# Kernel tuning notes

Measured on AMD Instinct MI355X. Metric: run time of the kernel, lower is better.

## Reference

```python
import jax, jax.numpy as jnp
import numpy as np

USER_NUM = 50000
ITEM_NUM = 50000
N = USER_NUM + ITEM_NUM
VT_DIM = 512
CAT_NUM = 1000
CAT_DIM = 32
HIDDEN = 128
OUT = 64
E = 2_000_000
BAG = 5


def setup_inputs() -> dict:
    key = jax.random.key(0)
    ks = jax.random.split(key, 12)
    inp = {
        "vt_feature": jax.random.normal(ks[0], (ITEM_NUM, VT_DIM), jnp.float32),
        "cat_indices": jax.random.randint(ks[1], (ITEM_NUM * BAG,), 0, CAT_NUM),
        "cat_offsets": jnp.arange(ITEM_NUM) * BAG,
        "edge_index": jax.random.randint(ks[2], (2, E), 0, N),
        # learned parameters
        "cat_table": jax.random.normal(ks[3], (CAT_NUM, CAT_DIM), jnp.float32) * 0.1,
        "fuse_w": jax.random.normal(ks[4], (HIDDEN, VT_DIM + CAT_DIM), jnp.float32) * (1.0 / np.sqrt(VT_DIM + CAT_DIM)),
        "user": jax.random.normal(ks[5], (USER_NUM, HIDDEN), jnp.float32) * 0.1,
        "w1_l": jax.random.normal(ks[6], (HIDDEN, HIDDEN), jnp.float32) * (1.0 / np.sqrt(HIDDEN)),
        "b1": jnp.zeros((HIDDEN,), jnp.float32),
        "w1_r": jax.random.normal(ks[7], (HIDDEN, HIDDEN), jnp.float32) * (1.0 / np.sqrt(HIDDEN)),
        "w2_l": jax.random.normal(ks[8], (OUT, HIDDEN), jnp.float32) * (1.0 / np.sqrt(HIDDEN)),
        "b2": jnp.zeros((OUT,), jnp.float32),
        "w2_r": jax.random.normal(ks[9], (OUT, HIDDEN), jnp.float32) * (1.0 / np.sqrt(HIDDEN)),
    }
    return inp


def _embedding_bag_mean(table, indices, offsets, num_bags):
    # EmbeddingBag(mode='mean') with offsets: segment-mean of table lookups.
    pos = jnp.arange(indices.shape[0])
    seg = jnp.searchsorted(offsets, pos, side="right") - 1  # bag id per index
    sums = jax.ops.segment_sum(table[indices], seg, num_segments=num_bags)
    cnt = jax.ops.segment_sum(jnp.ones_like(pos, jnp.float32), seg, num_segments=num_bags)
    return sums / jnp.maximum(cnt, 1.0)[:, None]


def _sage_conv(x, edge_index, w_l, b_l, w_r):
    # PyG SAGEConv (aggr='mean'): lin_l(mean_{j->i} x_j) + lin_r(x_i)
    src, dst = edge_index[0], edge_index[1]
    agg = jax.ops.segment_sum(x[src], dst, num_segments=N)
    deg = jax.ops.segment_sum(jnp.ones((src.shape[0],), x.dtype), dst, num_segments=N)
    agg = agg / jnp.maximum(deg, 1.0)[:, None]
    return agg @ w_l.T + b_l + x @ w_r.T


def reference(vt_feature, cat_indices, cat_offsets, edge_index, cat_table,
              fuse_w, user, w1_l, b1, w1_r, w2_l, b2, w2_r):
    cat_emb = _embedding_bag_mean(cat_table, cat_indices, cat_offsets, ITEM_NUM)
    item_feat = jnp.concatenate([vt_feature, cat_emb], axis=1) @ fuse_w.T
    x0 = jnp.concatenate([user, item_feat], axis=0)  # [N, hidden]
    x1 = jax.nn.leaky_relu(_sage_conv(x0, edge_index, w1_l, b1, w1_r), negative_slope=0.01)
    # dropout is identity in eval mode
    x2 = _sage_conv(x1, edge_index, w2_l, b2, w2_r)
    return x2
```

## Files before the change

### kernel.cpp

```cpp
#include <hip/hip_runtime.h>

#define USER_N   50000
#define ITEM_N   50000
#define NNODE    100000
#define VT_DIM   512
#define CAT_DIM  32
#define HIDDEN   128
#define OUTD     64
#define PADCAP   64

#define BINC    8192
#define NBKT    98
#define BSHIFT  10
#define SLICES  8

typedef __attribute__((ext_vector_type(8))) short short8;
typedef __attribute__((ext_vector_type(4))) float f32x4;

__device__ __forceinline__ float bf2f(unsigned short u) {
    return __uint_as_float(((unsigned int)u) << 16);
}
__device__ __forceinline__ unsigned short f2bf(float f) {
    unsigned int u = __float_as_uint(f);
    unsigned int r = u + 0x7fffu + ((u >> 16) & 1u);
    return (unsigned short)(r >> 16);
}

__global__ __launch_bounds__(256) void k_catemb(const float* __restrict__ cat_table,
                                                const int* __restrict__ cat_idx,
                                                const int* __restrict__ cat_off,
                                                unsigned short* __restrict__ catemb,
                                                int item_num, int total_idx) {
    int gid = blockIdx.x * 256 + threadIdx.x;
    int item = gid >> 5;
    int d = gid & 31;
    if (item >= item_num) return;
    int s = cat_off[item];
    int e = (item + 1 < item_num) ? cat_off[item + 1] : total_idx;
    float acc = 0.f;
    for (int j = s; j < e; ++j) {
        int idx = cat_idx[j];
        acc += cat_table[idx * CAT_DIM + d];
    }
    int cnt = e - s;
    float inv = 1.f / (float)(cnt > 0 ? cnt : 1);
    catemb[(size_t)item * CAT_DIM + d] = f2bf(acc * inv);
}

__global__ __launch_bounds__(256) void k_copy_user(const float* __restrict__ user,
                                                   unsigned short* __restrict__ x0, int n4) {
    int gid = blockIdx.x * 256 + threadIdx.x;
    if (gid >= n4) return;
    float4 v = ((const float4*)user)[gid];
    ushort4 o;
    o.x = f2bf(v.x); o.y = f2bf(v.y); o.z = f2bf(v.z); o.w = f2bf(v.w);
    ((ushort4*)x0)[gid] = o;
}

#define ASTR 40

__global__ __launch_bounds__(256, 2) void k_fuse_mfma(const float* __restrict__ vt,
                                                      const unsigned short* __restrict__ catemb,
                                                      const float* __restrict__ fw,
                                                      unsigned short* __restrict__ x0) {
    __shared__ __align__(16) unsigned short Al[256 * ASTR];
    __shared__ __align__(16) unsigned short Bl[128 * ASTR];
    int tid = threadIdx.x;
    int wave = tid >> 6, lane = tid & 63, quad = lane >> 4, l16 = lane & 15;
    int br0 = blockIdx.x * 256;
    int arow = br0 + tid;

    f32x4 acc[4][8];
#pragma unroll
    for (int m = 0; m < 4; m++)
#pragma unroll
        for (int n = 0; n < 8; n++) acc[m][n] = (f32x4){0.f, 0.f, 0.f, 0.f};

    for (int kb = 0; kb < 17; ++kb) {
        if (kb < 16) {
            if (arow < ITEM_N) {
                const float* src = vt + (size_t)arow * VT_DIM + kb * 32;
#pragma unroll
                for (int i = 0; i < 8; i++) {
                    float4 v = ((const float4*)src)[i];
                    ushort4 o;
                    o.x = f2bf(v.x); o.y = f2bf(v.y); o.z = f2bf(v.z); o.w = f2bf(v.w);
                    *(ushort4*)&Al[tid * ASTR + i * 4] = o;
                }
            } else {
                ushort4 z = {0, 0, 0, 0};
#pragma unroll
                for (int i = 0; i < 8; i++) *(ushort4*)&Al[tid * ASTR + i * 4] = z;
            }
        } else {
            if (arow < ITEM_N) {
                const uint4* src = (const uint4*)(catemb + (size_t)arow * CAT_DIM);
                *(uint4*)&Al[tid * ASTR]      = src[0];
                *(uint4*)&Al[tid * ASTR + 8]  = src[1];
                *(uint4*)&Al[tid * ASTR + 16] = src[2];
                *(uint4*)&Al[tid * ASTR + 24] = src[3];
            } else {
                uint4 z = {0, 0, 0, 0};
                *(uint4*)&Al[tid * ASTR]      = z;
                *(uint4*)&Al[tid * ASTR + 8]  = z;
                *(uint4*)&Al[tid * ASTR + 16] = z;
                *(uint4*)&Al[tid * ASTR + 24] = z;
            }
        }
        {
            int n = tid & 127, kh = tid >> 7;
            const float* src = fw + (size_t)n * (VT_DIM + CAT_DIM) + kb * 32 + kh * 16;
#pragma unroll
            for (int i = 0; i < 4; i++) {
                float4 v = ((const float4*)src)[i];
                ushort4 o;
                o.x = f2bf(v.x); o.y = f2bf(v.y); o.z = f2bf(v.z); o.w = f2bf(v.w);
                *(ushort4*)&Bl[n * ASTR + kh * 16 + i * 4] = o;
            }
        }
        __syncthreads();
        short8 av[4];
#pragma unroll
        for (int m = 0; m < 4; m++)
            av[m] = *(const short8*)&Al[(wave * 64 + m * 16 + l16) * ASTR + quad * 8];
#pragma unroll
        for (int nf = 0; nf < 8; nf++) {
            short8 bv = *(const short8*)&Bl[(nf * 16 + l16) * ASTR + quad * 8];
#pragma unroll
            for (int m = 0; m < 4; m++)
                acc[m][nf] = __builtin_amdgcn_mfma_f32_16x16x32_bf16(av[m], bv, acc[m][nf], 0, 0, 0);
        }
        __syncthreads();
    }
    int rbase = br0 + wave * 64;
#pragma unroll
    for (int m = 0; m < 4; m++) {
#pragma unroll
        for (int r = 0; r < 4; r++) {
            int row = rbase + m * 16 + quad * 4 + r;
            if (row < ITEM_N) {
#pragma unroll
                for (int nf = 0; nf < 8; nf++) {
                    int col = nf * 16 + l16;
                    x0[(size_t)(USER_N + row) * HIDDEN + col] = f2bf(acc[m][nf][r]);
                }
            }
        }
    }
}

__global__ __launch_bounds__(256, 2) void k_l1_mfma(const unsigned short* __restrict__ agg1,
                                                    const unsigned short* __restrict__ x0,
                                                    const float* __restrict__ w1l,
                                                    const float* __restrict__ w1r,
                                                    const float* __restrict__ b1,
                                                    unsigned short* __restrict__ x1) {
    __shared__ __align__(16) unsigned short Al[256 * ASTR];
    __shared__ __align__(16) unsigned short Bl[128 * ASTR];
    int tid = threadIdx.x;
    int wave = tid >> 6, lane = tid & 63, quad = lane >> 4, l16 = lane & 15;
    int br0 = blockIdx.x * 256;
    int arow = br0 + tid;

    f32x4 acc[4][8];
#pragma unroll
    for (int m = 0; m < 4; m++)
#pragma unroll
        for (int n = 0; n < 8; n++) acc[m][n] = (f32x4){0.f, 0.f, 0.f, 0.f};

    for (int kb = 0; kb < 8; ++kb) {
        const unsigned short* abase = (kb < 4) ? agg1 : x0;
        int kc = (kb & 3) * 32;
        if (arow < NNODE) {
            const uint4* src = (const uint4*)(abase + (size_t)arow * HIDDEN + kc);
            *(uint4*)&Al[tid * ASTR]      = src[0];
            *(uint4*)&Al[tid * ASTR + 8]  = src[1];
            *(uint4*)&Al[tid * ASTR + 16] = src[2];
            *(uint4*)&Al[tid * ASTR + 24] = src[3];
        } else {
            uint4 z = {0, 0, 0, 0};
            *(uint4*)&Al[tid * ASTR]      = z;
            *(uint4*)&Al[tid * ASTR + 8]  = z;
            *(uint4*)&Al[tid * ASTR + 16] = z;
            *(uint4*)&Al[tid * ASTR + 24] = z;
        }
        {
            int n = tid & 127, kh = tid >> 7;
            const float* src = ((kb < 4) ? w1l : w1r) + (size_t)n * HIDDEN + kc + kh * 16;
#pragma unroll
            for (int i = 0; i < 4; i++) {
                float4 v = ((const float4*)src)[i];
                ushort4 o;
                o.x = f2bf(v.x); o.y = f2bf(v.y); o.z = f2bf(v.z); o.w = f2bf(v.w);
                *(ushort4*)&Bl[n * ASTR + kh * 16 + i * 4] = o;
            }
        }
        __syncthreads();
        short8 av[4];
#pragma unroll
        for (int m = 0; m < 4; m++)
            av[m] = *(const short8*)&Al[(wave * 64 + m * 16 + l16) * ASTR + quad * 8];
#pragma unroll
        for (int nf = 0; nf < 8; nf++) {
            short8 bv = *(const short8*)&Bl[(nf * 16 + l16) * ASTR + quad * 8];
#pragma unroll
            for (int m = 0; m < 4; m++)
                acc[m][nf] = __builtin_amdgcn_mfma_f32_16x16x32_bf16(av[m], bv, acc[m][nf], 0, 0, 0);
        }
        __syncthreads();
    }
    float bias[8];
#pragma unroll
    for (int nf = 0; nf < 8; nf++) bias[nf] = b1[nf * 16 + l16];
    int rbase = br0 + wave * 64;
#pragma unroll
    for (int m = 0; m < 4; m++) {
#pragma unroll
        for (int r = 0; r < 4; r++) {
            int row = rbase + m * 16 + quad * 4 + r;
            if (row < NNODE) {
#pragma unroll
                for (int nf = 0; nf < 8; nf++) {
                    int col = nf * 16 + l16;
                    float v = acc[m][nf][r] + bias[nf];
                    v = (v >= 0.f) ? v : 0.01f * v;
                    x1[(size_t)row * HIDDEN + col] = f2bf(v);
                }
            }
        }
    }
}

__global__ __launch_bounds__(256, 2) void k_l2_mfma(const unsigned short* __restrict__ x1,
                                                    const float* __restrict__ w2l,
                                                    const float* __restrict__ w2r,
                                                    const float* __restrict__ b2,
                                                    unsigned short* __restrict__ y1,
                                                    float* __restrict__ outw) {
    __shared__ __align__(16) unsigned short Al[256 * ASTR];
    __shared__ __align__(16) unsigned short Bl[128 * ASTR];
    int tid = threadIdx.x;
    int wave = tid >> 6, lane = tid & 63, quad = lane >> 4, l16 = lane & 15;
    int br0 = blockIdx.x * 256;
    int arow = br0 + tid;

    f32x4 acc[4][8];
#pragma unroll
    for (int m = 0; m < 4; m++)
#pragma unroll
        for (int n = 0; n < 8; n++) acc[m][n] = (f32x4){0.f, 0.f, 0.f, 0.f};

    for (int kb = 0; kb < 4; ++kb) {
        int kc = kb * 32;
        if (arow < NNODE) {
            const uint4* src = (const uint4*)(x1 + (size_t)arow * HIDDEN + kc);
            *(uint4*)&Al[tid * ASTR]      = src[0];
            *(uint4*)&Al[tid * ASTR + 8]  = src[1];
            *(uint4*)&Al[tid * ASTR + 16] = src[2];
            *(uint4*)&Al[tid * ASTR + 24] = src[3];
        } else {
            uint4 z = {0, 0, 0, 0};
            *(uint4*)&Al[tid * ASTR]      = z;
            *(uint4*)&Al[tid * ASTR + 8]  = z;
            *(uint4*)&Al[tid * ASTR + 16] = z;
            *(uint4*)&Al[tid * ASTR + 24] = z;
        }
        {
            int n = tid & 127, kh = tid >> 7;
            const float* wsrc = (n < 64) ? (w2l + (size_t)n * HIDDEN)
                                         : (w2r + (size_t)(n - 64) * HIDDEN);
            const float* src = wsrc + kc + kh * 16;
#pragma unroll
            for (int i = 0; i < 4; i++) {
                float4 v = ((const float4*)src)[i];
                ushort4 o;
                o.x = f2bf(v.x); o.y = f2bf(v.y); o.z = f2bf(v.z); o.w = f2bf(v.w);
                *(ushort4*)&Bl[n * ASTR + kh * 16 + i * 4] = o;
            }
        }
        __syncthreads();
        short8 av[4];
#pragma unroll
        for (int m = 0; m < 4; m++)
            av[m] = *(const short8*)&Al[(wave * 64 + m * 16 + l16) * ASTR + quad * 8];
#pragma unroll
        for (int nf = 0; nf < 8; nf++) {
            short8 bv = *(const short8*)&Bl[(nf * 16 + l16) * ASTR + quad * 8];
#pragma unroll
            for (int m = 0; m < 4; m++)
                acc[m][nf] = __builtin_amdgcn_mfma_f32_16x16x32_bf16(av[m], bv, acc[m][nf], 0, 0, 0);
        }
        __syncthreads();
    }
    float bias2[4];
#pragma unroll
    for (int nf = 0; nf < 4; nf++) bias2[nf] = b2[nf * 16 + l16];
    int rbase = br0 + wave * 64;
#pragma unroll
    for (int m = 0; m < 4; m++) {
#pragma unroll
        for (int r = 0; r < 4; r++) {
            int row = rbase + m * 16 + quad * 4 + r;
            if (row < NNODE) {
#pragma unroll
                for (int nf = 0; nf < 4; nf++) {
                    int col = nf * 16 + l16;
                    y1[(size_t)row * OUTD + col] = f2bf(acc[m][nf][r]);
                }
#pragma unroll
                for (int nf = 4; nf < 8; nf++) {
                    int col = (nf - 4) * 16 + l16;
                    outw[(size_t)row * OUTD + col] = acc[m][nf][r] + bias2[nf - 4];
                }
            }
        }
    }
}

__global__ __launch_bounds__(256) void k_deg(const int* __restrict__ dst, int ne4, int ne, int* __restrict__ deg) {
    int t = blockIdx.x * 256 + threadIdx.x;
    int base = t * 4;
    if (t < ne4) {
        int4 d4 = *(const int4*)&dst[base];
        atomicAdd(&deg[d4.x], 1);
        atomicAdd(&deg[d4.y], 1);
        atomicAdd(&deg[d4.z], 1);
        atomicAdd(&deg[d4.w], 1);
    } else {
        for (int e = base; e < ne; ++e) atomicAdd(&deg[dst[e]], 1);
    }
}

__global__ __launch_bounds__(256) void k_scanA(const int* __restrict__ deg, int n, int* __restrict__ bsum) {
    __shared__ int sd[256];
    int i = blockIdx.x * 256 + threadIdx.x;
    sd[threadIdx.x] = (i < n) ? deg[i] : 0;
    __syncthreads();
    for (int o = 128; o > 0; o >>= 1) {
        if (threadIdx.x < o) sd[threadIdx.x] += sd[threadIdx.x + o];
        __syncthreads();
    }
    if (threadIdx.x == 0) bsum[blockIdx.x] = sd[0];
}

__global__ __launch_bounds__(512) void k_scanB(const int* __restrict__ bsum, int nb, int* __restrict__ boff) {
    __shared__ int sd[512];
    int t = threadIdx.x;
    int v = (t < nb) ? bsum[t] : 0;
    sd[t] = v;
    __syncthreads();
    for (int o = 1; o < 512; o <<= 1) {
        int x = 0;
        if (t >= o) x = sd[t - o];
        __syncthreads();
        sd[t] += x;
        __syncthreads();
    }
    if (t < nb) boff[t] = sd[t] - v;
}

__global__ __launch_bounds__(256) void k_scanC(const int* __restrict__ deg, int n,
                                               const int* __restrict__ boff,
                                               int* __restrict__ offs, int* __restrict__ cursor, int ne) {
    __shared__ int sd[256];
    int i = blockIdx.x * 256 + threadIdx.x;
    int v = (i < n) ? deg[i] : 0;
    sd[threadIdx.x] = v;
    __syncthreads();
    for (int o = 1; o < 256; o <<= 1) {
        int x = 0;
        if (threadIdx.x >= o) x = sd[threadIdx.x - o];
        __syncthreads();
        sd[threadIdx.x] += x;
        __syncthreads();
    }
    if (i < n) {
        int ex = boff[blockIdx.x] + sd[threadIdx.x] - v;
        offs[i] = ex;
        cursor[i] = ex;
    }
    if (i == 0) offs[n] = ne;
}

__global__ __launch_bounds__(256) void k_scatter(const int* __restrict__ src, const int* __restrict__ dst,
                                                 int ne4, int ne, int* __restrict__ cursor, int* __restrict__ csr) {
    int t = blockIdx.x * 256 + threadIdx.x;
    int base = t * 4;
    if (t < ne4) {
        int4 d4 = *(const int4*)&dst[base];
        int4 s4 = *(const int4*)&src[base];
        int p0 = atomicAdd(&cursor[d4.x], 1);
        int p1 = atomicAdd(&cursor[d4.y], 1);
        int p2 = atomicAdd(&cursor[d4.z], 1);
        int p3 = atomicAdd(&cursor[d4.w], 1);
        csr[p0] = s4.x;
        csr[p1] = s4.y;
        csr[p2] = s4.z;
        csr[p3] = s4.w;
    } else {
        for (int e = base; e < ne; ++e) {
            int slot = atomicAdd(&cursor[dst[e]], 1);
            csr[slot] = src[e];
        }
    }
}

__global__ __launch_bounds__(256) void k_scatter_pad(const int* __restrict__ src, const int* __restrict__ dst,
                                                     int ne4, int ne, int* __restrict__ cursor,
                                                     int* __restrict__ csrp) {
    int t = blockIdx.x * 256 + threadIdx.x;
    int base = t * 4;
    if (t < ne4) {
        int4 d4 = *(const int4*)&dst[base];
        int4 s4 = *(const int4*)&src[base];
        int p0 = atomicAdd(&cursor[d4.x], 1);
        int p1 = atomicAdd(&cursor[d4.y], 1);
        int p2 = atomicAdd(&cursor[d4.z], 1);
        int p3 = atomicAdd(&cursor[d4.w], 1);
        if (p0 < PADCAP) csrp[d4.x * PADCAP + p0] = s4.x;
        if (p1 < PADCAP) csrp[d4.y * PADCAP + p1] = s4.y;
        if (p2 < PADCAP) csrp[d4.z * PADCAP + p2] = s4.z;
        if (p3 < PADCAP) csrp[d4.w * PADCAP + p3] = s4.w;
    } else {
        for (int e = base; e < ne; ++e) {
            int d = dst[e];
            int slot = atomicAdd(&cursor[d], 1);
            if (slot < PADCAP) csrp[d * PADCAP + slot] = src[e];
        }
    }
}

__global__ __launch_bounds__(256) void k_hist(const int* __restrict__ dst, int ne,
                                              int nblk, int* __restrict__ hist) {
    __shared__ int lh[NBKT];
    int b = blockIdx.x;
    for (int i = threadIdx.x; i < NBKT; i += 256) lh[i] = 0;
    __syncthreads();
    int s = b * BINC;
    int e = (s + BINC < ne) ? (s + BINC) : ne;
    for (int j = s + threadIdx.x; j < e; j += 256) {
        atomicAdd(&lh[dst[j] >> BSHIFT], 1);
    }
    __syncthreads();
    for (int i = threadIdx.x; i < NBKT; i += 256) hist[i * nblk + b] = lh[i];
}

__global__ __launch_bounds__(1024) void k_scan1(int* __restrict__ hist, int tot) {
    __shared__ int ls[1024];
    int t = threadIdx.x;
    int K = (tot + 1023) >> 10;
    int base = t * K;
    int end = base + K;
    if (end > tot) end = tot;
    int s = 0;
    for (int i = base; i < end; ++i) s += hist[i];
    ls[t] = s;
    __syncthreads();
    for (int o = 1; o < 1024; o <<= 1) {
        int v = (t >= o) ? ls[t - o] : 0;
        __syncthreads();
        ls[t] += v;
        __syncthreads();
    }
    int run = ls[t] - s;
    for (int i = base; i < end; ++i) {
        int tmp = hist[i];
        hist[i] = run;
        run += tmp;
    }
}

__global__ __launch_bounds__(256) void k_binscatter(const int* __restrict__ src,
                                                    const int* __restrict__ dst,
                                                    int ne, int nblk,
                                                    const int* __restrict__ hist,
                                                    int2* __restrict__ ebin) {
    __shared__ int lc[NBKT];
    int b = blockIdx.x;
    for (int i = threadIdx.x; i < NBKT; i += 256) lc[i] = hist[i * nblk + b];
    __syncthreads();
    int s = b * BINC;
    int e = (s + BINC < ne) ? (s + BINC) : ne;
    for (int j = s + threadIdx.x; j < e; j += 256) {
        int d = dst[j];
        int p = atomicAdd(&lc[d >> BSHIFT], 1);
        ebin[p] = make_int2(src[j], d);
    }
}

__global__ __launch_bounds__(256) void k_scatter_bkt(const int2* __restrict__ ebin,
                                                     const int* __restrict__ hist,
                                                     int nblk, int ne,
                                                     int* __restrict__ cursor,
                                                     int* __restrict__ csrp) {
    int xcd = blockIdx.x & 7;
    int w = blockIdx.x >> 3;
    int i = w / SLICES, sl = w - i * SLICES;
    int b = xcd + (i << 3);
    if (b >= NBKT) return;
    int s0 = hist[b * nblk];
    int e0 = (b + 1 < NBKT) ? hist[(b + 1) * nblk] : ne;
    int len = e0 - s0;
    int per = (len + SLICES - 1) / SLICES;
    int s = s0 + sl * per;
    int e = (s + per < e0) ? (s + per) : e0;
    for (int j = s + threadIdx.x; j < e; j += 256) {
        int2 p = ebin[j];
        int slot = atomicAdd(&cursor[p.y], 1);
        if (slot < PADCAP) csrp[p.y * PADCAP + slot] = p.x;
    }
}

__global__ __launch_bounds__(256) void k_agg1(const unsigned short* __restrict__ x0,
                                              const int* __restrict__ offs,
                                              const int* __restrict__ cnts,
                                              int pad,
                                              const int* __restrict__ csr,
                                              unsigned short* __restrict__ agg1) {
    int wid = (blockIdx.x << 2) + (threadIdx.x >> 6);
    if (wid >= NNODE) return;
    int lane = threadIdx.x & 63;
    int half = lane >> 5;
    int l32 = lane & 31;
    int s, e, d;
    if (pad) {
        s = wid << 6;
        int c = cnts[wid];
        d = c;
        e = s + (c < PADCAP ? c : PADCAP);
    } else {
        s = offs[wid];
        e = offs[wid + 1];
        d = e - s;
    }
    float a0 = 0.f, a1 = 0.f, a2 = 0.f, a3 = 0.f;
    int j = s;
    for (; j + 16 <= e; j += 16) {
        int sn[8];
#pragma unroll
        for (int u = 0; u < 8; u++) sn[u] = csr[j + 2 * u + half];
        ushort4 v[8];
#pragma unroll
        for (int u = 0; u < 8; u++) v[u] = *(const ushort4*)&x0[(size_t)sn[u] * HIDDEN + l32 * 4];
#pragma unroll
        for (int u = 0; u < 8; u++) {
            a0 += bf2f(v[u].x);
            a1 += bf2f(v[u].y);
            a2 += bf2f(v[u].z);
            a3 += bf2f(v[u].w);
        }
    }
    for (; j + 8 <= e; j += 8) {
        int sn0 = csr[j     + half];
        int sn1 = csr[j + 2 + half];
        int sn2 = csr[j + 4 + half];
        int sn3 = csr[j + 6 + half];
        ushort4 v0 = *(const ushort4*)&x0[(size_t)sn0 * HIDDEN + l32 * 4];
        ushort4 v1 = *(const ushort4*)&x0[(size_t)sn1 * HIDDEN + l32 * 4];
        ushort4 v2 = *(const ushort4*)&x0[(size_t)sn2 * HIDDEN + l32 * 4];
        ushort4 v3 = *(const ushort4*)&x0[(size_t)sn3 * HIDDEN + l32 * 4];
        a0 += bf2f(v0.x) + bf2f(v1.x) + bf2f(v2.x) + bf2f(v3.x);
        a1 += bf2f(v0.y) + bf2f(v1.y) + bf2f(v2.y) + bf2f(v3.y);
        a2 += bf2f(v0.z) + bf2f(v1.z) + bf2f(v2.z) + bf2f(v3.z);
        a3 += bf2f(v0.w) + bf2f(v1.w) + bf2f(v2.w) + bf2f(v3.w);
    }
    for (; j < e; j += 2) {
        int myj = j + half;
        bool ok = (myj < e);
        int sn = ok ? csr[myj] : csr[j];
        float w = ok ? 1.f : 0.f;
        ushort4 v = *(const ushort4*)&x0[(size_t)sn * HIDDEN + l32 * 4];
        a0 += w * bf2f(v.x);
        a1 += w * bf2f(v.y);
        a2 += w * bf2f(v.z);
        a3 += w * bf2f(v.w);
    }
    a0 += __shfl_xor(a0, 32, 64);
    a1 += __shfl_xor(a1, 32, 64);
    a2 += __shfl_xor(a2, 32, 64);
    a3 += __shfl_xor(a3, 32, 64);
    float inv = 1.f / (float)(d > 0 ? d : 1);
    if (half == 0) {
        ushort4 o;
        o.x = f2bf(a0 * inv);
        o.y = f2bf(a1 * inv);
        o.z = f2bf(a2 * inv);
        o.w = f2bf(a3 * inv);
        *(ushort4*)&agg1[(size_t)wid * HIDDEN + l32 * 4] = o;
    }
}

__global__ __launch_bounds__(256) void k_agg2_out(const unsigned short* __restrict__ y1,
                                                  const int* __restrict__ offs,
                                                  const int* __restrict__ cnts,
                                                  int pad,
                                                  const int* __restrict__ csr,
                                                  float* __restrict__ out) {
    int wid = (blockIdx.x << 2) + (threadIdx.x >> 6);
    if (wid >= NNODE) return;
    int lane = threadIdx.x & 63;
    int quad = lane >> 4;
    int l16 = lane & 15;
    int s, e, d;
    if (pad) {
        s = wid << 6;
        int c = cnts[wid];
        d = c;
        e = s + (c < PADCAP ? c : PADCAP);
    } else {
        s = offs[wid];
        e = offs[wid + 1];
        d = e - s;
    }
    float a0 = 0.f, a1 = 0.f, a2 = 0.f, a3 = 0.f;
    int j = s;
    for (; j + 16 <= e; j += 16) {
        int sn0 = csr[j      + quad];
        int sn1 = csr[j + 4  + quad];
        int sn2 = csr[j + 8  + quad];
        int sn3 = csr[j + 12 + quad];
        ushort4 v0 = *(const ushort4*)&y1[(size_t)sn0 * OUTD + l16 * 4];
        ushort4 v1 = *(const ushort4*)&y1[(size_t)sn1 * OUTD + l16 * 4];
        ushort4 v2 = *(const ushort4*)&y1[(size_t)sn2 * OUTD + l16 * 4];
        ushort4 v3 = *(const ushort4*)&y1[(size_t)sn3 * OUTD + l16 * 4];
        a0 += bf2f(v0.x) + bf2f(v1.x) + bf2f(v2.x) + bf2f(v3.x);
        a1 += bf2f(v0.y) + bf2f(v1.y) + bf2f(v2.y) + bf2f(v3.y);
        a2 += bf2f(v0.z) + bf2f(v1.z) + bf2f(v2.z) + bf2f(v3.z);
        a3 += bf2f(v0.w) + bf2f(v1.w) + bf2f(v2.w) + bf2f(v3.w);
    }
    for (; j < e; j += 4) {
        int myj = j + quad;
        bool ok = (myj < e);
        int sn = ok ? csr[myj] : csr[j];
        float w = ok ? 1.f : 0.f;
        ushort4 v = *(const ushort4*)&y1[(size_t)sn * OUTD + l16 * 4];
        a0 += w * bf2f(v.x);
        a1 += w * bf2f(v.y);
        a2 += w * bf2f(v.z);
        a3 += w * bf2f(v.w);
    }
    a0 += __shfl_xor(a0, 16, 64);
    a1 += __shfl_xor(a1, 16, 64);
    a2 += __shfl_xor(a2, 16, 64);
    a3 += __shfl_xor(a3, 16, 64);
    a0 += __shfl_xor(a0, 32, 64);
    a1 += __shfl_xor(a1, 32, 64);
    a2 += __shfl_xor(a2, 32, 64);
    a3 += __shfl_xor(a3, 32, 64);
    float inv = 1.f / (float)(d > 0 ? d : 1);
    if (quad == 0) {
        float4* op = (float4*)&out[(size_t)wid * OUTD + l16 * 4];
        float4 prev = *op;
        float4 o;
        o.x = a0 * inv + prev.x;
        o.y = a1 * inv + prev.y;
        o.z = a2 * inv + prev.z;
        o.w = a3 * inv + prev.w;
        *op = o;
    }
}

extern "C" void kernel_launch(void* const* d_in, const int* in_sizes, int n_in,
                              void* d_out, int out_size, void* d_ws, size_t ws_size,
                              hipStream_t stream) {
    const float* vt      = (const float*)d_in[0];
    const int*   cat_idx = (const int*)d_in[1];
    const int*   cat_off = (const int*)d_in[2];
    const int*   ei      = (const int*)d_in[3];
    const float* cat_tab = (const float*)d_in[4];
    const float* fuse_w  = (const float*)d_in[5];
    const float* user    = (const float*)d_in[6];
    const float* w1l     = (const float*)d_in[7];
    const float* b1      = (const float*)d_in[8];
    const float* w1r     = (const float*)d_in[9];
    const float* w2l     = (const float*)d_in[10];
    const float* b2      = (const float*)d_in[11];
    const float* w2r     = (const float*)d_in[12];
    float* out = (float*)d_out;

    const int ne = in_sizes[3] / 2;
    const int ne4 = ne / 4;
    const int total_idx = in_sizes[1];
    const int* esrc = ei;
    const int* edst = ei + ne;

    const size_t SZ_X0  = (size_t)NNODE * HIDDEN * 2;
    const size_t SZ_PAD = (size_t)NNODE * PADCAP * 4;
    const size_t SZ_CSR = (size_t)ne * 4;
    const size_t SZ_INT = (size_t)NNODE * 4;

    size_t need_pad = SZ_X0 * 3 + SZ_PAD + SZ_INT + 8192;
    size_t need_csr = SZ_X0 * 3 + SZ_CSR + SZ_INT * 3 + 4 * 4096 + 4096;

    char* p = (char*)d_ws;
    auto alloc = [&](size_t bytes) {
        char* q = p;
        p += (bytes + 255) & ~(size_t)255;
        return q;
    };

    const int nscan = (NNODE + 255) / 256;
    const int sc_blocks = (ne4 + 255) / 256;

    if (ws_size >= need_pad) {
        unsigned short* x0   = (unsigned short*)alloc(SZ_X0);
        unsigned short* aggY = (unsigned short*)alloc(SZ_X0);
        unsigned short* x1   = (unsigned short*)alloc(SZ_X0);
        int*            csrp = (int*)alloc(SZ_PAD);
        int*          cursor = (int*)alloc(SZ_INT);
        unsigned short* catemb = (unsigned short*)csrp;

        k_catemb<<<(ITEM_N * 32 + 255) / 256, 256, 0, stream>>>(cat_tab, cat_idx, cat_off, catemb, ITEM_N, total_idx);
        k_copy_user<<<(USER_N * HIDDEN / 4 + 255) / 256, 256, 0, stream>>>(user, x0, USER_N * HIDDEN / 4);
        k_fuse_mfma<<<(ITEM_N + 255) / 256, 256, 0, stream>>>(vt, catemb, fuse_w, x0);

        hipMemsetAsync(cursor, 0, SZ_INT, stream);

        const int nblk = (ne + BINC - 1) / BINC;
        bool fast_bin = ((size_t)ne * sizeof(int2) <= SZ_X0) &&
                        ((size_t)NBKT * nblk * sizeof(int) <= SZ_X0);
        if (fast_bin) {
            int*  hist = (int*)aggY;
            int2* ebin = (int2*)x1;
            k_hist<<<nblk, 256, 0, stream>>>(edst, ne, nblk, hist);
            k_scan1<<<1, 1024, 0, stream>>>(hist, NBKT * nblk);
            k_binscatter<<<nblk, 256, 0, stream>>>(esrc, edst, ne, nblk, hist, ebin);
            k_scatter_bkt<<<8 * 13 * SLICES, 256, 0, stream>>>(ebin, hist, nblk, ne, cursor, csrp);
        } else {
            k_scatter_pad<<<sc_blocks, 256, 0, stream>>>(esrc, edst, ne4, ne, cursor, csrp);
        }

        k_agg1<<<(NNODE + 3) / 4, 256, 0, stream>>>(x0, cursor, cursor, 1, csrp, aggY);
        k_l1_mfma<<<(NNODE + 255) / 256, 256, 0, stream>>>(aggY, x0, w1l, w1r, b1, x1);
        k_l2_mfma<<<(NNODE + 255) / 256, 256, 0, stream>>>(x1, w2l, w2r, b2, aggY, out);
        k_agg2_out<<<(NNODE + 3) / 4, 256, 0, stream>>>(aggY, cursor, cursor, 1, csrp, out);
    } else if (ws_size >= need_csr) {
        unsigned short* x0   = (unsigned short*)alloc(SZ_X0);
        unsigned short* aggY = (unsigned short*)alloc(SZ_X0);
        unsigned short* x1   = (unsigned short*)alloc(SZ_X0);
        char*           R4   = (char*)alloc(SZ_CSR);
        int* deg    = (int*)alloc(SZ_INT);
        int* offs   = (int*)alloc(SZ_INT + 256);
        int* cursor = (int*)alloc(SZ_INT);
        int* bsum   = (int*)alloc(512 * 4);
        int* boff   = (int*)alloc(512 * 4);
        unsigned short* catemb = (unsigned short*)R4;
        int*            csr    = (int*)R4;

        k_catemb<<<(ITEM_N * 32 + 255) / 256, 256, 0, stream>>>(cat_tab, cat_idx, cat_off, catemb, ITEM_N, total_idx);
        k_copy_user<<<(USER_N * HIDDEN / 4 + 255) / 256, 256, 0, stream>>>(user, x0, USER_N * HIDDEN / 4);
        k_fuse_mfma<<<(ITEM_N + 255) / 256, 256, 0, stream>>>(vt, catemb, fuse_w, x0);

        hipMemsetAsync(deg, 0, SZ_INT, stream);
        k_deg<<<sc_blocks, 256, 0, stream>>>(edst, ne4, ne, deg);
        k_scanA<<<nscan, 256, 0, stream>>>(deg, NNODE, bsum);
        k_scanB<<<1, 512, 0, stream>>>(bsum, nscan, boff);
        k_scanC<<<nscan, 256, 0, stream>>>(deg, NNODE, boff, offs, cursor, ne);
        k_scatter<<<sc_blocks, 256, 0, stream>>>(esrc, edst, ne4, ne, cursor, csr);

        k_agg1<<<(NNODE + 3) / 4, 256, 0, stream>>>(x0, offs, offs, 0, csr, aggY);
        k_l1_mfma<<<(NNODE + 255) / 256, 256, 0, stream>>>(aggY, x0, w1l, w1r, b1, x1);
        k_l2_mfma<<<(NNODE + 255) / 256, 256, 0, stream>>>(x1, w2l, w2r, b2, aggY, out);
        k_agg2_out<<<(NNODE + 3) / 4, 256, 0, stream>>>(aggY, offs, offs, 0, csr, out);
    } else {
        hipMemsetAsync(d_out, 0, (size_t)out_size * 4, stream);
    }
}
```

Baseline: 536.8 us.

## Shrink MFMA GEMM row tiles to 64 and widen gather loads to 16 bytes

The three dense MFMA GEMM kernels now use 64-row tiles per block instead of 256, with four times as many blocks and a higher occupancy hint. This is meant to fill the GPU better, at the cost of reloading the weight tile into shared memory more often. The two neighbour-aggregation kernels are rewritten to load 8 bf16 values per lane with 16-byte loads and to spread edges across more lane groups, reducing gather instruction count and improving memory-level parallelism.

After: 550.4 us. 2.5% more time.

```diff
diff --git a/kernel.cpp b/kernel.cpp
--- a/kernel.cpp
+++ b/kernel.cpp
@@ -24,6 +24,29 @@
     unsigned int u = __float_as_uint(f);
     unsigned int r = u + 0x7fffu + ((u >> 16) & 1u);
     return (unsigned short)(r >> 16);
+}
+__device__ __forceinline__ unsigned int pk2(float lo, float hi) {
+    return ((unsigned int)f2bf(hi) << 16) | (unsigned int)f2bf(lo);
+}
+__device__ __forceinline__ void acc8(float* a, uint4 v) {
+    a[0] += __uint_as_float(v.x << 16);
+    a[1] += __uint_as_float(v.x & 0xffff0000u);
+    a[2] += __uint_as_float(v.y << 16);
+    a[3] += __uint_as_float(v.y & 0xffff0000u);
+    a[4] += __uint_as_float(v.z << 16);
+    a[5] += __uint_as_float(v.z & 0xffff0000u);
+    a[6] += __uint_as_float(v.w << 16);
+    a[7] += __uint_as_float(v.w & 0xffff0000u);
+}
+__device__ __forceinline__ void acc8w(float* a, uint4 v, float w) {
+    a[0] += w * __uint_as_float(v.x << 16);
+    a[1] += w * __uint_as_float(v.x & 0xffff0000u);
+    a[2] += w * __uint_as_float(v.y << 16);
+    a[3] += w * __uint_as_float(v.y & 0xffff0000u);
+    a[4] += w * __uint_as_float(v.z << 16);
+    a[5] += w * __uint_as_float(v.z & 0xffff0000u);
+    a[6] += w * __uint_as_float(v.w << 16);
+    a[7] += w * __uint_as_float(v.w & 0xffff0000u);
 }
 
 __global__ __launch_bounds__(256) void k_catemb(const float* __restrict__ cat_table,
@@ -59,52 +82,45 @@
 
 #define ASTR 40
 
-__global__ __launch_bounds__(256, 2) void k_fuse_mfma(const float* __restrict__ vt,
+__global__ __launch_bounds__(256, 4) void k_fuse_mfma(const float* __restrict__ vt,
                                                       const unsigned short* __restrict__ catemb,
                                                       const float* __restrict__ fw,
                                                       unsigned short* __restrict__ x0) {
-    __shared__ __align__(16) unsigned short Al[256 * ASTR];
+    __shared__ __align__(16) unsigned short Al[64 * ASTR];
     __shared__ __align__(16) unsigned short Bl[128 * ASTR];
     int tid = threadIdx.x;
     int wave = tid >> 6, lane = tid & 63, quad = lane >> 4, l16 = lane & 15;
-    int br0 = blockIdx.x * 256;
-    int arow = br0 + tid;
-
-    f32x4 acc[4][8];
-#pragma unroll
-    for (int m = 0; m < 4; m++)
-#pragma unroll
-        for (int n = 0; n < 8; n++) acc[m][n] = (f32x4){0.f, 0.f, 0.f, 0.f};
+    int br0 = blockIdx.x * 64;
+    int row = tid >> 2, q4 = tid & 3;
+    int arow = br0 + row;
+
+    f32x4 acc[8];
+#pragma unroll
+    for (int n = 0; n < 8; n++) acc[n] = (f32x4){0.f, 0.f, 0.f, 0.f};
 
     for (int kb = 0; kb < 17; ++kb) {
         if (kb < 16) {
             if (arow < ITEM_N) {
-                const float* src = vt + (size_t)arow * VT_DIM + kb * 32;
-#pragma unroll
-                for (int i = 0; i < 8; i++) {
-                    float4 v = ((const float4*)src)[i];
-                    ushort4 o;
-                    o.x = f2bf(v.x); o.y = f2bf(v.y); o.z = f2bf(v.z); o.w = f2bf(v.w);
-                    *(ushort4*)&Al[tid * ASTR + i * 4] = o;
-                }
+                const float* src = vt + (size_t)arow * VT_DIM + kb * 32 + q4 * 8;
+                float4 v0 = ((const float4*)src)[0];
+                float4 v1 = ((const float4*)src)[1];
+                ushort4 o0, o1;
+                o0.x = f2bf(v0.x); o0.y = f2bf(v0.y); o0.z = f2bf(v0.z); o0.w = f2bf(v0.w);
+                o1.x = f2bf(v1.x); o1.y = f2bf(v1.y); o1.z = f2bf(v1.z); o1.w = f2bf(v1.w);
+                *(ushort4*)&Al[row * ASTR + q4 * 8]     = o0;
+                *(ushort4*)&Al[row * ASTR + q4 * 8 + 4] = o1;
             } else {
                 ushort4 z = {0, 0, 0, 0};
-#pragma unroll
-                for (int i = 0; i < 8; i++) *(ushort4*)&Al[tid * ASTR + i * 4] = z;
+                *(ushort4*)&Al[row * ASTR + q4 * 8]     = z;
+                *(ushort4*)&Al[row * ASTR + q4 * 8 + 4] = z;
             }
         } else {
             if (arow < ITEM_N) {
-                const uint4* src = (const uint4*)(catemb + (size_t)arow * CAT_DIM);
-                *(uint4*)&Al[tid * ASTR]      = src[0];
-                *(uint4*)&Al[tid * ASTR + 8]  = src[1];
-                *(uint4*)&Al[tid * ASTR + 16] = src[2];
-                *(uint4*)&Al[tid * ASTR + 24] = src[3];
+                uint4 v = *(const uint4*)(catemb + (size_t)arow * CAT_DIM + q4 * 8);
+                *(uint4*)&Al[row * ASTR + q4 * 8] = v;
             } else {
                 uint4 z = {0, 0, 0, 0};
-                *(uint4*)&Al[tid * ASTR]      = z;
-                *(uint4*)&Al[tid * ASTR + 8]  = z;
-                *(uint4*)&Al[tid * ASTR + 16] = z;
-                *(uint4*)&Al[tid * ASTR + 24] = z;
+                *(uint4*)&Al[row * ASTR + q4 * 8] = z;
             }
         }
         {
@@ -119,70 +135,55 @@
             }
         }
         __syncthreads();
-        short8 av[4];
-#pragma unroll
-        for (int m = 0; m < 4; m++)
-            av[m] = *(const short8*)&Al[(wave * 64 + m * 16 + l16) * ASTR + quad * 8];
+        short8 av = *(const short8*)&Al[(wave * 16 + l16) * ASTR + quad * 8];
 #pragma unroll
         for (int nf = 0; nf < 8; nf++) {
             short8 bv = *(const short8*)&Bl[(nf * 16 + l16) * ASTR + quad * 8];
-#pragma unroll
-            for (int m = 0; m < 4; m++)
-                acc[m][nf] = __builtin_amdgcn_mfma_f32_16x16x32_bf16(av[m], bv, acc[m][nf], 0, 0, 0);
-        }
-        __syncthreads();
-    }
-    int rbase = br0 + wave * 64;
-#pragma unroll
-    for (int m = 0; m < 4; m++) {
-#pragma unroll
-        for (int r = 0; r < 4; r++) {
-            int row = rbase + m * 16 + quad * 4 + r;
-            if (row < ITEM_N) {
-#pragma unroll
-                for (int nf = 0; nf < 8; nf++) {
-                    int col = nf * 16 + l16;
-                    x0[(size_t)(USER_N + row) * HIDDEN + col] = f2bf(acc[m][nf][r]);
-                }
-            }
-        }
-    }
-}
-
-__global__ __launch_bounds__(256, 2) void k_l1_mfma(const unsigned short* __restrict__ agg1,
+            acc[nf] = __builtin_amdgcn_mfma_f32_16x16x32_bf16(av, bv, acc[nf], 0, 0, 0);
+        }
+        __syncthreads();
+    }
+    int rbase = br0 + wave * 16 + quad * 4;
+#pragma unroll
+    for (int r = 0; r < 4; r++) {
+        int orow = rbase + r;
+        if (orow < ITEM_N) {
+#pragma unroll
+            for (int nf = 0; nf < 8; nf++) {
+                int col = nf * 16 + l16;
+                x0[(size_t)(USER_N + orow) * HIDDEN + col] = f2bf(acc[nf][r]);
+            }
+        }
+    }
+}
+
+__global__ __launch_bounds__(256, 4) void k_l1_mfma(const unsigned short* __restrict__ agg1,
                                                     const unsigned short* __restrict__ x0,
                                                     const float* __restrict__ w1l,
                                                     const float* __restrict__ w1r,
                                                     const float* __restrict__ b1,
                                                     unsigned short* __restrict__ x1) {
-    __shared__ __align__(16) unsigned short Al[256 * ASTR];
+    __shared__ __align__(16) unsigned short Al[64 * ASTR];
     __shared__ __align__(16) unsigned short Bl[128 * ASTR];
     int tid = threadIdx.x;
     int wave = tid >> 6, lane = tid & 63, quad = lane >> 4, l16 = lane & 15;
-    int br0 = blockIdx.x * 256;
-    int arow = br0 + tid;
-
-    f32x4 acc[4][8];
-#pragma unroll
-    for (int m = 0; m < 4; m++)
-#pragma unroll
-        for (int n = 0; n < 8; n++) acc[m][n] = (f32x4){0.f, 0.f, 0.f, 0.f};
+    int br0 = blockIdx.x * 64;
+    int row = tid >> 2, q4 = tid & 3;
+    int arow = br0 + row;
+
+    f32x4 acc[8];
+#pragma unroll
+    for (int n = 0; n < 8; n++) acc[n] = (f32x4){0.f, 0.f, 0.f, 0.f};
 
     for (int kb = 0; kb < 8; ++kb) {
         const unsigned short* abase = (kb < 4) ? agg1 : x0;
         int kc = (kb & 3) * 32;
         if (arow < NNODE) {
-            const uint4* src = (const uint4*)(abase + (size_t)arow * HIDDEN + kc);
-            *(uint4*)&Al[tid * ASTR]      = src[0];
-            *(uint4*)&Al[tid * ASTR + 8]  = src[1];
-            *(uint4*)&Al[tid * ASTR + 16] = src[2];
-            *(uint4*)&Al[tid * ASTR + 24] = src[3];
+            uint4 v = *(const uint4*)(abase + (size_t)arow * HIDDEN + kc + q4 * 8);
+            *(uint4*)&Al[row * ASTR + q4 * 8] = v;
         } else {
             uint4 z = {0, 0, 0, 0};
-            *(uint4*)&Al[tid * ASTR]      = z;
-            *(uint4*)&Al[tid * ASTR + 8]  = z;
-            *(uint4*)&Al[tid * ASTR + 16] = z;
-            *(uint4*)&Al[tid * ASTR + 24] = z;
+            *(uint4*)&Al[row * ASTR + q4 * 8] = z;
         }
         {
             int n = tid & 127, kh = tid >> 7;
@@ -196,74 +197,59 @@
             }
         }
         __syncthreads();
-        short8 av[4];
-#pragma unroll
-        for (int m = 0; m < 4; m++)
-            av[m] = *(const short8*)&Al[(wave * 64 + m * 16 + l16) * ASTR + quad * 8];
+        short8 av = *(const short8*)&Al[(wave * 16 + l16) * ASTR + quad * 8];
 #pragma unroll
         for (int nf = 0; nf < 8; nf++) {
             short8 bv = *(const short8*)&Bl[(nf * 16 + l16) * ASTR + quad * 8];
-#pragma unroll
-            for (int m = 0; m < 4; m++)
-                acc[m][nf] = __builtin_amdgcn_mfma_f32_16x16x32_bf16(av[m], bv, acc[m][nf], 0, 0, 0);
+            acc[nf] = __builtin_amdgcn_mfma_f32_16x16x32_bf16(av, bv, acc[nf], 0, 0, 0);
         }
         __syncthreads();
     }
     float bias[8];
 #pragma unroll
     for (int nf = 0; nf < 8; nf++) bias[nf] = b1[nf * 16 + l16];
-    int rbase = br0 + wave * 64;
-#pragma unroll
-    for (int m = 0; m < 4; m++) {
-#pragma unroll
-        for (int r = 0; r < 4; r++) {
-            int row = rbase + m * 16 + quad * 4 + r;
-            if (row < NNODE) {
-#pragma unroll
-                for (int nf = 0; nf < 8; nf++) {
-                    int col = nf * 16 + l16;
-                    float v = acc[m][nf][r] + bias[nf];
-                    v = (v >= 0.f) ? v : 0.01f * v;
-                    x1[(size_t)row * HIDDEN + col] = f2bf(v);
-                }
-            }
-        }
-    }
-}
-
-__global__ __launch_bounds__(256, 2) void k_l2_mfma(const unsigned short* __restrict__ x1,
+    int rbase = br0 + wave * 16 + quad * 4;
+#pragma unroll
+    for (int r = 0; r < 4; r++) {
+        int orow = rbase + r;
+        if (orow < NNODE) {
+#pragma unroll
+            for (int nf = 0; nf < 8; nf++) {
+                int col = nf * 16 + l16;
+                float v = acc[nf][r] + bias[nf];
+                v = (v >= 0.f) ? v : 0.01f * v;
+                x1[(size_t)orow * HIDDEN + col] = f2bf(v);
+            }
+        }
+    }
+}
+
+__global__ __launch_bounds__(256, 4) void k_l2_mfma(const unsigned short* __restrict__ x1,
                                                     const float* __restrict__ w2l,
                                                     const float* __restrict__ w2r,
                                                     const float* __restrict__ b2,
                                                     unsigned short* __restrict__ y1,
                                                     float* __restrict__ outw) {
-    __shared__ __align__(16) unsigned short Al[256 * ASTR];
+    __shared__ __align__(16) unsigned short Al[64 * ASTR];
     __shared__ __align__(16) unsigned short Bl[128 * ASTR];
     int tid = threadIdx.x;
     int wave = tid >> 6, lane = tid & 63, quad = lane >> 4, l16 = lane & 15;
-    int br0 = blockIdx.x * 256;
-    int arow = br0 + tid;
-
-    f32x4 acc[4][8];
-#pragma unroll
-    for (int m = 0; m < 4; m++)
-#pragma unroll
-        for (int n = 0; n < 8; n++) acc[m][n] = (f32x4){0.f, 0.f, 0.f, 0.f};
+    int br0 = blockIdx.x * 64;
+    int row = tid >> 2, q4 = tid & 3;
+    int arow = br0 + row;
+
+    f32x4 acc[8];
+#pragma unroll
+    for (int n = 0; n < 8; n++) acc[n] = (f32x4){0.f, 0.f, 0.f, 0.f};
 
     for (int kb = 0; kb < 4; ++kb) {
         int kc = kb * 32;
         if (arow < NNODE) {
-            const uint4* src = (const uint4*)(x1 + (size_t)arow * HIDDEN + kc);
-            *(uint4*)&Al[tid * ASTR]      = src[0];
-            *(uint4*)&Al[tid * ASTR + 8]  = src[1];
-            *(uint4*)&Al[tid * ASTR + 16] = src[2];
-            *(uint4*)&Al[tid * ASTR + 24] = src[3];
+            uint4 v = *(const uint4*)(x1 + (size_t)arow * HIDDEN + kc + q4 * 8);
+            *(uint4*)&Al[row * ASTR + q4 * 8] = v;
         } else {
             uint4 z = {0, 0, 0, 0};
-            *(uint4*)&Al[tid * ASTR]      = z;
-            *(uint4*)&Al[tid * ASTR + 8]  = z;
-            *(uint4*)&Al[tid * ASTR + 16] = z;
-            *(uint4*)&Al[tid * ASTR + 24] = z;
+            *(uint4*)&Al[row * ASTR + q4 * 8] = z;
         }
         {
             int n = tid & 127, kh = tid >> 7;
@@ -279,39 +265,31 @@
             }
         }
         __syncthreads();
-        short8 av[4];
-#pragma unroll
-        for (int m = 0; m < 4; m++)
-            av[m] = *(const short8*)&Al[(wave * 64 + m * 16 + l16) * ASTR + quad * 8];
+        short8 av = *(const short8*)&Al[(wave * 16 + l16) * ASTR + quad * 8];
 #pragma unroll
         for (int nf = 0; nf < 8; nf++) {
             short8 bv = *(const short8*)&Bl[(nf * 16 + l16) * ASTR + quad * 8];
-#pragma unroll
-            for (int m = 0; m < 4; m++)
-                acc[m][nf] = __builtin_amdgcn_mfma_f32_16x16x32_bf16(av[m], bv, acc[m][nf], 0, 0, 0);
+            acc[nf] = __builtin_amdgcn_mfma_f32_16x16x32_bf16(av, bv, acc[nf], 0, 0, 0);
         }
         __syncthreads();
     }
     float bias2[4];
 #pragma unroll
     for (int nf = 0; nf < 4; nf++) bias2[nf] = b2[nf * 16 + l16];
-    int rbase = br0 + wave * 64;
-#pragma unroll
-    for (int m = 0; m < 4; m++) {
-#pragma unroll
-        for (int r = 0; r < 4; r++) {
-            int row = rbase + m * 16 + quad * 4 + r;
-            if (row < NNODE) {
-#pragma unroll
-                for (int nf = 0; nf < 4; nf++) {
-                    int col = nf * 16 + l16;
-                    y1[(size_t)row * OUTD + col] = f2bf(acc[m][nf][r]);
-                }
-#pragma unroll
-                for (int nf = 4; nf < 8; nf++) {
-                    int col = (nf - 4) * 16 + l16;
-                    outw[(size_t)row * OUTD + col] = acc[m][nf][r] + bias2[nf - 4];
-                }
+    int rbase = br0 + wave * 16 + quad * 4;
+#pragma unroll
+    for (int r = 0; r < 4; r++) {
+        int orow = rbase + r;
+        if (orow < NNODE) {
+#pragma unroll
+            for (int nf = 0; nf < 4; nf++) {
+                int col = nf * 16 + l16;
+                y1[(size_t)orow * OUTD + col] = f2bf(acc[nf][r]);
+            }
+#pragma unroll
+            for (int nf = 4; nf < 8; nf++) {
+                int col = (nf - 4) * 16 + l16;
+                outw[(size_t)orow * OUTD + col] = acc[nf][r] + bias2[nf - 4];
             }
         }
     }
@@ -520,85 +498,6 @@
     int wid = (blockIdx.x << 2) + (threadIdx.x >> 6);
     if (wid >= NNODE) return;
     int lane = threadIdx.x & 63;
-    int half = lane >> 5;
-    int l32 = lane & 31;
-    int s, e, d;
-    if (pad) {
-        s = wid << 6;
-        int c = cnts[wid];
-        d = c;
-        e = s + (c < PADCAP ? c : PADCAP);
-    } else {
-        s = offs[wid];
-        e = offs[wid + 1];
-        d = e - s;
-    }
-    float a0 = 0.f, a1 = 0.f, a2 = 0.f, a3 = 0.f;
-    int j = s;
-    for (; j + 16 <= e; j += 16) {
-        int sn[8];
-#pragma unroll
-        for (int u = 0; u < 8; u++) sn[u] = csr[j + 2 * u + half];
-        ushort4 v[8];
-#pragma unroll
-        for (int u = 0; u < 8; u++) v[u] = *(const ushort4*)&x0[(size_t)sn[u] * HIDDEN + l32 * 4];
-#pragma unroll
-        for (int u = 0; u < 8; u++) {
-            a0 += bf2f(v[u].x);
-            a1 += bf2f(v[u].y);
-            a2 += bf2f(v[u].z);
-            a3 += bf2f(v[u].w);
-        }
-    }
-    for (; j + 8 <= e; j += 8) {
-        int sn0 = csr[j     + half];
-        int sn1 = csr[j + 2 + half];
-        int sn2 = csr[j + 4 + half];
-        int sn3 = csr[j + 6 + half];
-        ushort4 v0 = *(const ushort4*)&x0[(size_t)sn0 * HIDDEN + l32 * 4];
-        ushort4 v1 = *(const ushort4*)&x0[(size_t)sn1 * HIDDEN + l32 * 4];
-        ushort4 v2 = *(const ushort4*)&x0[(size_t)sn2 * HIDDEN + l32 * 4];
-        ushort4 v3 = *(const ushort4*)&x0[(size_t)sn3 * HIDDEN + l32 * 4];
-        a0 += bf2f(v0.x) + bf2f(v1.x) + bf2f(v2.x) + bf2f(v3.x);
-        a1 += bf2f(v0.y) + bf2f(v1.y) + bf2f(v2.y) + bf2f(v3.y);
-        a2 += bf2f(v0.z) + bf2f(v1.z) + bf2f(v2.z) + bf2f(v3.z);
-        a3 += bf2f(v0.w) + bf2f(v1.w) + bf2f(v2.w) + bf2f(v3.w);
-    }
-    for (; j < e; j += 2) {
-        int myj = j + half;
-        bool ok = (myj < e);
-        int sn = ok ? csr[myj] : csr[j];
-        float w = ok ? 1.f : 0.f;
-        ushort4 v = *(const ushort4*)&x0[(size_t)sn * HIDDEN + l32 * 4];
-        a0 += w * bf2f(v.x);
-        a1 += w * bf2f(v.y);
-        a2 += w * bf2f(v.z);
-        a3 += w * bf2f(v.w);
-    }
-    a0 += __shfl_xor(a0, 32, 64);
-    a1 += __shfl_xor(a1, 32, 64);
-    a2 += __shfl_xor(a2, 32, 64);
-    a3 += __shfl_xor(a3, 32, 64);
-    float inv = 1.f / (float)(d > 0 ? d : 1);
-    if (half == 0) {
-        ushort4 o;
-        o.x = f2bf(a0 * inv);
-        o.y = f2bf(a1 * inv);
-        o.z = f2bf(a2 * inv);
-        o.w = f2bf(a3 * inv);
-        *(ushort4*)&agg1[(size_t)wid * HIDDEN + l32 * 4] = o;
-    }
-}
-
-__global__ __launch_bounds__(256) void k_agg2_out(const unsigned short* __restrict__ y1,
-                                                  const int* __restrict__ offs,
-                                                  const int* __restrict__ cnts,
-                                                  int pad,
-                                                  const int* __restrict__ csr,
-                                                  float* __restrict__ out) {
-    int wid = (blockIdx.x << 2) + (threadIdx.x >> 6);
-    if (wid >= NNODE) return;
-    int lane = threadIdx.x & 63;
     int quad = lane >> 4;
     int l16 = lane & 15;
     int s, e, d;
@@ -612,51 +511,104 @@
         e = offs[wid + 1];
         d = e - s;
     }
-    float a0 = 0.f, a1 = 0.f, a2 = 0.f, a3 = 0.f;
+    float a[8];
+#pragma unroll
+    for (int i = 0; i < 8; i++) a[i] = 0.f;
     int j = s;
     for (; j + 16 <= e; j += 16) {
         int sn0 = csr[j      + quad];
         int sn1 = csr[j + 4  + quad];
         int sn2 = csr[j + 8  + quad];
         int sn3 = csr[j + 12 + quad];
-        ushort4 v0 = *(const ushort4*)&y1[(size_t)sn0 * OUTD + l16 * 4];
-        ushort4 v1 = *(const ushort4*)&y1[(size_t)sn1 * OUTD + l16 * 4];
-        ushort4 v2 = *(const ushort4*)&y1[(size_t)sn2 * OUTD + l16 * 4];
-        ushort4 v3 = *(const ushort4*)&y1[(size_t)sn3 * OUTD + l16 * 4];
-        a0 += bf2f(v0.x) + bf2f(v1.x) + bf2f(v2.x) + bf2f(v3.x);
-        a1 += bf2f(v0.y) + bf2f(v1.y) + bf2f(v2.y) + bf2f(v3.y);
-        a2 += bf2f(v0.z) + bf2f(v1.z) + bf2f(v2.z) + bf2f(v3.z);
-        a3 += bf2f(v0.w) + bf2f(v1.w) + bf2f(v2.w) + bf2f(v3.w);
+        uint4 v0 = *(const uint4*)&x0[(size_t)sn0 * HIDDEN + l16 * 8];
+        uint4 v1 = *(const uint4*)&x0[(size_t)sn1 * HIDDEN + l16 * 8];
+        uint4 v2 = *(const uint4*)&x0[(size_t)sn2 * HIDDEN + l16 * 8];
+        uint4 v3 = *(const uint4*)&x0[(size_t)sn3 * HIDDEN + l16 * 8];
+        acc8(a, v0); acc8(a, v1); acc8(a, v2); acc8(a, v3);
     }
     for (; j < e; j += 4) {
         int myj = j + quad;
         bool ok = (myj < e);
-        int sn = ok ? csr[myj] : csr[j];
+        int sn = ok ? csr[myj] : csr[s];
         float w = ok ? 1.f : 0.f;
-        ushort4 v = *(const ushort4*)&y1[(size_t)sn * OUTD + l16 * 4];
-        a0 += w * bf2f(v.x);
-        a1 += w * bf2f(v.y);
-        a2 += w * bf2f(v.z);
-        a3 += w * bf2f(v.w);
-    }
-    a0 += __shfl_xor(a0, 16, 64);
-    a1 += __shfl_xor(a1, 16, 64);
-    a2 += __shfl_xor(a2, 16, 64);
-    a3 += __shfl_xor(a3, 16, 64);
-    a0 += __shfl_xor(a0, 32, 64);
-    a1 += __shfl_xor(a1, 32, 64);
-    a2 += __shfl_xor(a2, 32, 64);
-    a3 += __shfl_xor(a3, 32, 64);
+        uint4 v = *(const uint4*)&x0[(size_t)sn * HIDDEN + l16 * 8];
+        acc8w(a, v, w);
+    }
+#pragma unroll
+    for (int i = 0; i < 8; i++) {
+        a[i] += __shfl_xor(a[i], 16, 64);
+        a[i] += __shfl_xor(a[i], 32, 64);
+    }
     float inv = 1.f / (float)(d > 0 ? d : 1);
     if (quad == 0) {
-        float4* op = (float4*)&out[(size_t)wid * OUTD + l16 * 4];
-        float4 prev = *op;
-        float4 o;
-        o.x = a0 * inv + prev.x;
-        o.y = a1 * inv + prev.y;
-        o.z = a2 * inv + prev.z;
-        o.w = a3 * inv + prev.w;
-        *op = o;
+        uint4 o;
+        o.x = pk2(a[0] * inv, a[1] * inv);
+        o.y = pk2(a[2] * inv, a[3] * inv);
+        o.z = pk2(a[4] * inv, a[5] * inv);
+        o.w = pk2(a[6] * inv, a[7] * inv);
+        *(uint4*)&agg1[(size_t)wid * HIDDEN + l16 * 8] = o;
+    }
+}
+
+__global__ __launch_bounds__(256) void k_agg2_out(const unsigned short* __restrict__ y1,
+                                                  const int* __restrict__ offs,
+                                                  const int* __restrict__ cnts,
+                                                  int pad,
+                                                  const int* __restrict__ csr,
+                                                  float* __restrict__ out) {
+    int wid = (blockIdx.x << 2) + (threadIdx.x >> 6);
+    if (wid >= NNODE) return;
+    int lane = threadIdx.x & 63;
+    int oct = lane >> 3;
+    int l8 = lane & 7;
+    int s, e, d;
+    if (pad) {
+        s = wid << 6;
+        int c = cnts[wid];
+        d = c;
+        e = s + (c < PADCAP ? c : PADCAP);
+    } else {
+        s = offs[wid];
+        e = offs[wid + 1];
+        d = e - s;
+    }
+    float a[8];
+#pragma unroll
+    for (int i = 0; i < 8; i++) a[i] = 0.f;
+    int j = s;
+    for (; j + 16 <= e; j += 16) {
+        int sn0 = csr[j     + oct];
+        int sn1 = csr[j + 8 + oct];
+        uint4 v0 = *(const uint4*)&y1[(size_t)sn0 * OUTD + l8 * 8];
+        uint4 v1 = *(const uint4*)&y1[(size_t)sn1 * OUTD + l8 * 8];
+        acc8(a, v0); acc8(a, v1);
+    }
+    for (; j < e; j += 8) {
+        int myj = j + oct;
+        bool ok = (myj < e);
+        int sn = ok ? csr[myj] : csr[s];
+        float w = ok ? 1.f : 0.f;
+        uint4 v = *(const uint4*)&y1[(size_t)sn * OUTD + l8 * 8];
+        acc8w(a, v, w);
+    }
+#pragma unroll
+    for (int i = 0; i < 8; i++) {
+        a[i] += __shfl_xor(a[i], 8, 64);
+        a[i] += __shfl_xor(a[i], 16, 64);
+        a[i] += __shfl_xor(a[i], 32, 64);
+    }
+    float inv = 1.f / (float)(d > 0 ? d : 1);
+    if (oct == 0) {
+        float4* op = (float4*)&out[(size_t)wid * OUTD + l8 * 8];
+        float4 p0 = op[0];
+        float4 p1 = op[1];
+        float4 o0, o1;
+        o0.x = a[0] * inv + p0.x; o0.y = a[1] * inv + p0.y;
+        o0.z = a[2] * inv + p0.z; o0.w = a[3] * inv + p0.w;
+        o1.x = a[4] * inv + p1.x; o1.y = a[5] * inv + p1.y;
+        o1.z = a[6] * inv + p1.z; o1.w = a[7] * inv + p1.w;
+        op[0] = o0;
+        op[1] = o1;
     }
 }
 
@@ -712,7 +664,7 @@
 
         k_catemb<<<(ITEM_N * 32 + 255) / 256, 256, 0, stream>>>(cat_tab, cat_idx, cat_off, catemb, ITEM_N, total_idx);
         k_copy_user<<<(USER_N * HIDDEN / 4 + 255) / 256, 256, 0, stream>>>(user, x0, USER_N * HIDDEN / 4);
-        k_fuse_mfma<<<(ITEM_N + 255) / 256, 256, 0, stream>>>(vt, catemb, fuse_w, x0);
+        k_fuse_mfma<<<(ITEM_N + 63) / 64, 256, 0, stream>>>(vt, catemb, fuse_w, x0);
 
         hipMemsetAsync(cursor, 0, SZ_INT, stream);
 
@@ -731,8 +683,8 @@
         }
 
         k_agg1<<<(NNODE + 3) / 4, 256, 0, stream>>>(x0, cursor, cursor, 1, csrp, aggY);
-        k_l1_mfma<<<(NNODE + 255) / 256, 256, 0, stream>>>(aggY, x0, w1l, w1r, b1, x1);
-        k_l2_mfma<<<(NNODE + 255) / 256, 256, 0, stream>>>(x1, w2l, w2r, b2, aggY, out);
+        k_l1_mfma<<<(NNODE + 63) / 64, 256, 0, stream>>>(aggY, x0, w1l, w1r, b1, x1);
+        k_l2_mfma<<<(NNODE + 63) / 64, 256, 0, stream>>>(x1, w2l, w2r, b2, aggY, out);
         k_agg2_out<<<(NNODE + 3) / 4, 256, 0, stream>>>(aggY, cursor, cursor, 1, csrp, out);
     } else if (ws_size >= need_csr) {
         unsigned short* x0   = (unsigned short*)alloc(SZ_X0);
@@ -749,7 +701,7 @@
 
         k_catemb<<<(ITEM_N * 32 + 255) / 256, 256, 0, stream>>>(cat_tab, cat_idx, cat_off, catemb, ITEM_N, total_idx);
         k_copy_user<<<(USER_N * HIDDEN / 4 + 255) / 256, 256, 0, stream>>>(user, x0, USER_N * HIDDEN / 4);
-        k_fuse_mfma<<<(ITEM_N + 255) / 256, 256, 0, stream>>>(vt, catemb, fuse_w, x0);
+        k_fuse_mfma<<<(ITEM_N + 63) / 64, 256, 0, stream>>>(vt, catemb, fuse_w, x0);
 
         hipMemsetAsync(deg, 0, SZ_INT, stream);
         k_deg<<<sc_blocks, 256, 0, stream>>>(edst, ne4, ne, deg);
@@ -759,8 +711,8 @@
         k_scatter<<<sc_blocks, 256, 0, stream>>>(esrc, edst, ne4, ne, cursor, csr);
 
         k_agg1<<<(NNODE + 3) / 4, 256, 0, stream>>>(x0, offs, offs, 0, csr, aggY);
-        k_l1_mfma<<<(NNODE + 255) / 256, 256, 0, stream>>>(aggY, x0, w1l, w1r, b1, x1);
-        k_l2_mfma<<<(NNODE + 255) / 256, 256, 0, stream>>>(x1, w2l, w2r, b2, aggY, out);
+        k_l1_mfma<<<(NNODE + 63) / 64, 256, 0, stream>>>(aggY, x0, w1l, w1r, b1, x1);
+        k_l2_mfma<<<(NNODE + 63) / 64, 256, 0, stream>>>(x1, w2l, w2r, b2, aggY, out);
         k_agg2_out<<<(NNODE + 3) / 4, 256, 0, stream>>>(aggY, offs, offs, 0, csr, out);
     } else {
         hipMemsetAsync(d_out, 0, (size_t)out_size * 4, stream);
```
